# Optimization experiments

Hardware: AMD Instinct MI355X
Metric: run time of the kernel (lower is better)

The kernel has to match this reference:

```python
import jax, jax.numpy as jnp
import numpy as np

SC = 11  # window stride / block size; unfold kernel = 3*SC = 33, padding = SC


def _unfold3(x, sc):
    """Equivalent of nn.Unfold(kernel=3*sc, stride=sc, padding=sc) on [b,c,H,W]
    where H, W are multiples of sc. Returns [b, c, 9*sc*sc, n_windows].
    Patch ordering within K differs from torch by a fixed permutation, which is
    immaterial: all contractions over K (mask, softmax, value aggregation) are
    permutation-invariant as long as the same unfold is used everywhere."""
    b, c, H, W = x.shape
    h_sc, w_sc = H // sc, W // sc
    xp = jnp.pad(x, ((0, 0), (0, 0), (sc, sc), (sc, sc)))
    blk = xp.reshape(b, c, h_sc + 2, sc, w_sc + 2, sc)
    # 3x3 neighborhood of sc-blocks around each window
    pat = jnp.stack([blk[:, :, di:di + h_sc, :, dj:dj + w_sc, :]
                     for di in range(3) for dj in range(3)], axis=2)
    # [b,c,9,h_sc,r,w_sc,s] -> [b,c,9,r,s,h_sc,w_sc] -> [b,c,9*sc*sc,n]
    pat = pat.transpose(0, 1, 2, 4, 6, 3, 5)
    return pat.reshape(b, c, 9 * sc * sc, h_sc * w_sc)


def _block_q(x, sc):
    """view(b,c,h_sc,sc,w_sc,sc).permute(0,1,2,4,3,5) -> [b,c,n,sc*sc]"""
    b, c, H, W = x.shape
    h_sc, w_sc = H // sc, W // sc
    y = x.reshape(b, c, h_sc, sc, w_sc, sc).transpose(0, 1, 2, 4, 3, 5)
    return y.reshape(b, c, h_sc * w_sc, sc * sc)


def setup_inputs() -> dict:
    key = jax.random.key(0)
    k1, k2, k3, k4, k5, k6 = jax.random.split(key, 6)
    b, c, h, w = 2, 64, 256, 256
    s = 1.0 / np.sqrt(c)
    return {
        "x_key": jax.random.normal(k1, (b, c, h, w), jnp.float32),
        "x_ref": jax.random.normal(k2, (b, c, h, w), jnp.float32),
        "Wq": jax.random.normal(k3, (c, c), jnp.float32) * s,
        "Wk": jax.random.normal(k4, (c, c), jnp.float32) * s,
        "Wv": jax.random.normal(k5, (c, c), jnp.float32) * s,
        "gamma": jax.random.normal(k6, (1,), jnp.float32) * 0.1,
    }


def reference(x_key, x_ref, Wq, Wk, Wv, gamma):
    sc = SC
    b, c, h_in, w_in = x_key.shape
    x_pad = sc - w_in % sc
    y_pad = sc - h_in % sc
    pad = ((0, 0), (0, 0), (0, y_pad), (0, x_pad))
    fk = jnp.pad(x_key, pad)
    fr = jnp.pad(x_ref, pad)
    b, c, h, w = fk.shape
    h_sc, w_sc = h // sc, w // sc

    # validity mask -> additive attention bias (out-of-image keys penalized)
    fm = jnp.pad(jnp.ones((1, 1, h_in, w_in), fk.dtype), pad)
    fm_k = _unfold3(fm, sc)          # [1,1,K,n]
    fm_q = _block_q(fm, sc)          # [1,1,n,s]
    am = (jnp.einsum('bckn,bcns->bkns', fm_k, fm_q) - 1.0) * 99.0  # [1,K,n,s]

    scale = c ** (-0.5)
    q = jnp.einsum('oi,bihw->bohw', Wq, fk)
    k = jnp.einsum('oi,bihw->bohw', Wk, fr)
    v = jnp.einsum('oi,bihw->bohw', Wv, fr)

    k_u = _unfold3(k, sc) * scale    # [b,c,K,n]
    q_b = _block_q(q, sc)            # [b,c,n,s]
    attn = jnp.einsum('bckn,bcns->bkns', k_u, q_b) + am  # [b,K,n,s]
    attn = jax.nn.softmax(attn, axis=1)

    v_u = _unfold3(v, sc)            # [b,c,K,n]
    r = jnp.einsum('bkns,bckn->bcns', attn, v_u)  # [b,c,n,s]
    r = r.reshape(b, c, h_sc, w_sc, sc, sc).transpose(0, 1, 2, 4, 3, 5)
    r = r.reshape(b, c, h, w)[:, :, :h_in, :w_in]
    return x_ref + r * gamma[0]
```

## Files before the change

kernel.cpp:

```cpp
#include <hip/hip_runtime.h>


typedef unsigned short ushort_t;
typedef unsigned int   uint32;
typedef unsigned long long uint64;
typedef __attribute__((ext_vector_type(8))) short short8;
typedef __attribute__((ext_vector_type(4))) float f32x4;

#define MFMA16(a,b,c) __builtin_amdgcn_mfma_f32_16x16x32_bf16(a,b,c,0,0,0)

#if __has_builtin(__builtin_amdgcn_exp2f)
#define EXP2(x) __builtin_amdgcn_exp2f(x)
#else
#define EXP2(x) exp2f(x)
#endif
#if __has_builtin(__builtin_amdgcn_rcpf)
#define RCP(x) __builtin_amdgcn_rcpf(x)
#else
#define RCP(x) (1.0f/(x))
#endif

#define QPKT_OFF   0u
#define KPKT_OFF   18874368u
#define VPKT_OFF   37748736u

__device__ __forceinline__ ushort_t f2bf(float f){
  union { __bf16 h; ushort_t u; } c;
  c.h = (__bf16)f;
  return c.u;
}

__device__ __forceinline__ uint32 pkbf(float a, float b){
  union { __bf16 h[2]; uint32 u; } c;
  c.h[0] = (__bf16)a;
  c.h[1] = (__bf16)b;
  return c.u;
}

__device__ __forceinline__ void storeK8(ushort_t* __restrict__ base, int nt, int t,
                                        int l15, int h, f32x4 a){
  uint32 lo = pkbf(a[0], a[1]);
  uint32 hi = pkbf(a[2], a[3]);
  int lanep = l15 + 16*((2*t + (h>>1)) & 3);
  size_t off = (size_t)((nt*2 + (t>>1))*64 + lanep)*16 + 8*(h&1);
  *(uint2*)((char*)base + off) = make_uint2(lo, hi);
}

__device__ __forceinline__ short8 ldWfrag(const float* __restrict__ W, int t, int ks,
                                          int l15, int h, float scale){
  const float* p = W + (16*t + l15)*64 + 32*ks + 8*h;
  float4 a = *(const float4*)p;
  float4 b = *(const float4*)(p + 4);
  union { uint4 u; short8 s; } x;
  x.u.x = pkbf(a.x*scale, a.y*scale);
  x.u.y = pkbf(a.z*scale, a.w*scale);
  x.u.z = pkbf(b.x*scale, b.y*scale);
  x.u.w = pkbf(b.z*scale, b.w*scale);
  return x.s;
}

__global__ __launch_bounds__(256) void proj_kernel(
    const float* __restrict__ xk, const float* __restrict__ xr,
    const float* __restrict__ Wq, const float* __restrict__ Wk, const float* __restrict__ Wv,
    ushort_t* __restrict__ qpkt, ushort_t* __restrict__ kpkt, ushort_t* __restrict__ vpkt)
{
  __shared__ __align__(16) float sX[64*192];
  const int tid = threadIdx.x;
  const int lane = tid & 63, wv = tid >> 6;
  const int l15 = lane & 15, h = lane >> 4;
  const int bid = blockIdx.x;
  const bool isQ = bid >= 1152;
  const int id = isQ ? bid - 1152 : bid;
  const int b = id / 576, rem = id % 576, ty = rem / 24, tx = rem % 24;
  const float* xs = (isQ ? xk : xr) + (size_t)b*64*65536;
  const int oy = ty*11, ox = tx*11;
  const int ox3 = ox & 3, xa = ox - ox3;

  #pragma unroll
  for (int i = tid; i < 1024; i += 256) sX[(i>>4)*192 + 176 + (i&15)] = 0.f;

  {
    const int ch = tid >> 2, seg = tid & 3;
    const float* rowp = xs + (size_t)ch*65536 + (size_t)oy*256 + (xa + 4*seg);
    float* sdst = sX + ch*192 + 4*seg;
    if (ty < 23 && tx < 23){
      #pragma unroll
      for (int y = 0; y < 11; ++y)
        *(float4*)(sdst + y*16) = *(const float4*)(rowp + y*256);
    } else {
      const int xg = xa + 4*seg;
      #pragma unroll
      for (int y = 0; y < 11; ++y){
        const bool rk = (oy + y) < 256;
        float4 v;
        v.x = (rk && xg+0 < 256) ? rowp[y*256+0] : 0.f;
        v.y = (rk && xg+1 < 256) ? rowp[y*256+1] : 0.f;
        v.z = (rk && xg+2 < 256) ? rowp[y*256+2] : 0.f;
        v.w = (rk && xg+3 < 256) ? rowp[y*256+3] : 0.f;
        *(float4*)(sdst + y*16) = v;
      }
    }
  }
  __syncthreads();

  const f32x4 zero = {0.f, 0.f, 0.f, 0.f};
  #define XFL(nt, ks, dst) { \
    const int px_ = 16*(nt) + l15; \
    const int y_ = (px_*745) >> 13; \
    const float* pp_ = sX + (32*(ks) + 8*h)*192 + y_*16 + (px_ - y_*11) + ox3; \
    union { uint4 u; short8 s; } r_; \
    r_.u.x = pkbf(pp_[0],    pp_[192]); \
    r_.u.y = pkbf(pp_[384],  pp_[576]); \
    r_.u.z = pkbf(pp_[768],  pp_[960]); \
    r_.u.w = pkbf(pp_[1152], pp_[1344]); \
    dst = r_.s; }

  if (!isQ){
    short8 wkf[4][2], wvf[4][2];
    #pragma unroll
    for (int t = 0; t < 4; ++t){
      wkf[t][0] = ldWfrag(Wk, t, 0, l15, h, 1.f);  wkf[t][1] = ldWfrag(Wk, t, 1, l15, h, 1.f);
      wvf[t][0] = ldWfrag(Wv, t, 0, l15, h, 1.f);  wvf[t][1] = ldWfrag(Wv, t, 1, l15, h, 1.f);
    }
    ushort_t* kb = kpkt + (size_t)id*8192;
    ushort_t* vb = vpkt + (size_t)id*8192;
    const int nt0 = 2*wv, nt1 = 2*wv + 1;
    short8 xf0[2], xf1[2];
    XFL(nt0, 0, xf0[0]); XFL(nt0, 1, xf0[1]);
    XFL(nt1, 0, xf1[0]); XFL(nt1, 1, xf1[1]);
    #pragma unroll
    for (int t = 0; t < 4; ++t){
      f32x4 ak0 = MFMA16(wkf[t][0], xf0[0], zero); ak0 = MFMA16(wkf[t][1], xf0[1], ak0);
      f32x4 ak1 = MFMA16(wkf[t][0], xf1[0], zero); ak1 = MFMA16(wkf[t][1], xf1[1], ak1);
      f32x4 av0 = MFMA16(xf0[0], wvf[t][0], zero); av0 = MFMA16(xf0[1], wvf[t][1], av0);
      f32x4 av1 = MFMA16(xf1[0], wvf[t][0], zero); av1 = MFMA16(xf1[1], wvf[t][1], av1);
      storeK8(kb, nt0, t, l15, h, ak0);
      storeK8(kb, nt1, t, l15, h, ak1);
      uint4 pv;
      pv.x = pkbf(av0[0], av0[1]); pv.y = pkbf(av0[2], av0[3]);
      pv.z = pkbf(av1[0], av1[1]); pv.w = pkbf(av1[2], av1[3]);
      *(uint4*)((char*)vb + (size_t)((wv*4 + t)*64 + lane)*16) = pv;
    }
  } else {
    const float C1 = 0.18033688011112042f;
    short8 wqf[4][2];
    #pragma unroll
    for (int t = 0; t < 4; ++t){
      wqf[t][0] = ldWfrag(Wq, t, 0, l15, h, C1);  wqf[t][1] = ldWfrag(Wq, t, 1, l15, h, C1);
    }
    ushort_t* qb = qpkt + (size_t)id*8192;
    #pragma unroll
    for (int nn = 0; nn < 2; ++nn){
      const int nt = 2*wv + nn;
      short8 xf[2];
      XFL(nt, 0, xf[0]); XFL(nt, 1, xf[1]);
      #pragma unroll
      for (int t = 0; t < 4; ++t){
        f32x4 aq = MFMA16(wqf[t][0], xf[0], zero); aq = MFMA16(wqf[t][1], xf[1], aq);
        storeK8(qb, nt, t, l15, h, aq);
      }
    }
  }
  #undef XFL
}

__global__ __launch_bounds__(256) void attn_kernel(
    ushort_t* qpkt,
    const ushort_t* __restrict__ kpkt, const ushort_t* __restrict__ vpkt,
    const float* __restrict__ gamma)
{
  __shared__ __align__(16) char smem[49152];
  const int tid = threadIdx.x;
  const int lane = tid & 63, wave = tid >> 6;
  const int qh = wave & 1, kh = wave >> 1;
  const int win = (blockIdx.x & 7)*144 + (blockIdx.x >> 3);
  const int b = win / 576, wid = win % 576, wy = wid / 24, wx = wid % 24;
  const int l15 = lane & 15, h = lane >> 4;

  short8 qf[4][2];
  {
    const ushort_t* qblk = qpkt + (size_t)win*8192;
    #pragma unroll
    for (int mt = 0; mt < 4; ++mt){
      qf[mt][0] = *(const short8*)(qblk + (size_t)(((4*qh+mt)*2 + 0)*64 + lane)*8);
      qf[mt][1] = *(const short8*)(qblk + (size_t)(((4*qh+mt)*2 + 1)*64 + lane)*8);
    }
  }

  uint64 cks = 0; int nv = 0;
  #pragma unroll
  for (int ck = 0; ck < 9; ++ck){
    const int ty = wy - 1 + ck/3, tx = wx - 1 + ck%3;
    if ((unsigned)ty < 24u && (unsigned)tx < 24u){
      cks |= ((uint64)ck) << (4*nv); ++nv;
    }
  }
  const int nu = 2*nv;

  const f32x4 zz = {0.f,0.f,0.f,0.f};
  f32x4 o[4][4], lsumC[4];
  #pragma unroll
  for (int mt = 0; mt < 4; ++mt){
    lsumC[mt] = zz;
    #pragma unroll
    for (int u = 0; u < 4; ++u) o[mt][u] = zz;
  }
  f32x4 init_i;
  #pragma unroll
  for (int r = 0; r < 4; ++r) init_i[r] = (4*h + r >= 9) ? -1.0e4f : 0.f;
  short8 ones;
  #pragma unroll
  for (int j = 0; j < 8; ++j) ones[j] = (short)0x3F80;

  const ushort_t* gsrc = (wave < 2) ? kpkt : vpkt;
  const int ldsoff = (wave >> 1)*8192 + (wave & 1)*4096;

  #define STAGE(u, bo) { \
    const int t_ = (u) >> 1, hf_ = (u) & 1; \
    const int ck_ = (int)((cks >> (4*t_)) & 15); \
    const int cy_ = (ck_*11) >> 5; \
    const int ty_ = wy - 1 + cy_, tx_ = wx - 1 + (ck_ - 3*cy_); \
    const char* g_ = (const char*)(gsrc + (size_t)(b*576 + ty_*24 + tx_)*8192) \
                     + hf_*8192 + (wave & 1)*4096 + lane*16; \
    char* l_ = smem + (bo)*16384 + ldsoff + lane*16; \
    _Pragma("unroll") \
    for (int i_ = 0; i_ < 4; ++i_) \
      __builtin_amdgcn_global_load_lds( \
        (const __attribute__((address_space(1))) uint32*)(g_ + i_*1024), \
        (__attribute__((address_space(3))) uint32*)(l_ + i_*1024), 16, 0, 0); \
  }

  STAGE(0, 0);
  STAGE(1, 1);
  STAGE(2, 2);

  int bu = 0;
  #pragma unroll 1
  for (int u = 0; u < nu; ++u){
    const int remst = nu - 1 - u;
    if (remst >= 2)      { __asm__ volatile("s_waitcnt vmcnt(8)" ::: "memory"); }
    else if (remst == 1) { __asm__ volatile("s_waitcnt vmcnt(4)" ::: "memory"); }
    else                 { __asm__ volatile("s_waitcnt vmcnt(0)" ::: "memory"); }
    __builtin_amdgcn_s_barrier();
    __asm__ volatile("" ::: "memory");

    const int t = u >> 1, hf = u & 1;
    const int ckv = (int)((cks >> (4*t)) & 15);
    const int cyv = (ckv*11) >> 5;
    const int tyv = wy - 1 + cyv, txv = wx - 1 + (ckv - 3*cyv);
    const bool ey = (tyv == 23), ex = (txv == 23);
    const int ntp = 2*hf + kh;

    f32x4 b0, b1;
    if (ey | ex){
      #pragma unroll
      for (int kt = 0; kt < 2; ++kt){
        f32x4 bb;
        #pragma unroll
        for (int r = 0; r < 4; ++r){
          const int kl = 32*ntp + 16*kt + 4*h + r;
          const int ky = (kl*745) >> 13, kx = kl - ky*11;
          bool ok = (kl < 121) && (!ey || ky < 3) && (!ex || kx < 3);
          bb[r] = ok ? 0.f : -1.0e4f;
        }
        if (kt) b1 = bb; else b0 = bb;
      }
    } else {
      b0 = zz;
      b1 = (hf & kh) ? init_i : zz;
    }

    const char* lk = smem + bu*16384 + kh*4096;
    const char* lv = smem + bu*16384 + 8192 + kh*4096;
    short8 kf00 = *(const short8*)(lk + (0*64 + lane)*16);
    short8 kf01 = *(const short8*)(lk + (1*64 + lane)*16);
    short8 kf10 = *(const short8*)(lk + (2*64 + lane)*16);
    short8 kf11 = *(const short8*)(lk + (3*64 + lane)*16);
    short8 vf0  = *(const short8*)(lv + (0*64 + lane)*16);
    short8 vf1  = *(const short8*)(lv + (1*64 + lane)*16);
    short8 vf2  = *(const short8*)(lv + (2*64 + lane)*16);
    short8 vf3  = *(const short8*)(lv + (3*64 + lane)*16);

    __builtin_amdgcn_s_setprio(1);
    #pragma unroll
    for (int mt = 0; mt < 4; ++mt){
      f32x4 s0 = MFMA16(kf00, qf[mt][0], b0); s0 = MFMA16(kf01, qf[mt][1], s0);
      f32x4 s1 = MFMA16(kf10, qf[mt][0], b1); s1 = MFMA16(kf11, qf[mt][1], s1);
      float p[8];
      #pragma unroll
      for (int r = 0; r < 4; ++r){
        p[r]   = EXP2(s0[r]);
        p[4+r] = EXP2(s1[r]);
      }
      union { uint4 uu; short8 s; } af;
      af.uu.x = pkbf(p[0], p[1]); af.uu.y = pkbf(p[2], p[3]);
      af.uu.z = pkbf(p[4], p[5]); af.uu.w = pkbf(p[6], p[7]);
      o[mt][0] = MFMA16(af.s, vf0, o[mt][0]);
      o[mt][1] = MFMA16(af.s, vf1, o[mt][1]);
      o[mt][2] = MFMA16(af.s, vf2, o[mt][2]);
      o[mt][3] = MFMA16(af.s, vf3, o[mt][3]);
      lsumC[mt] = MFMA16(af.s, ones, lsumC[mt]);
    }
    __builtin_amdgcn_s_setprio(0);

    __asm__ volatile("" ::: "memory");
    __builtin_amdgcn_s_barrier();
    if (u + 3 < nu) STAGE(u + 3, bu);
    bu = (bu == 2) ? 0 : bu + 1;
  }
  #undef STAGE

  __syncthreads();
  {
    float* base = (float*)(smem + qh*12288);
    if (kh){
      #pragma unroll
      for (int mt = 0; mt < 4; ++mt){
        *(f32x4*)(base + (mt*2+0)*256 + lane*4) = o[mt][0];
        *(f32x4*)(base + (mt*2+1)*256 + lane*4) = o[mt][1];
        *(f32x4*)(base + (8+mt)*256 + lane*4)   = lsumC[mt];
      }
    }
  }
  __syncthreads();
  if (!kh){
    float* base = (float*)(smem + qh*12288);
    #pragma unroll
    for (int mt = 0; mt < 4; ++mt){
      o[mt][0] += *(const f32x4*)(base + (mt*2+0)*256 + lane*4);
      o[mt][1] += *(const f32x4*)(base + (mt*2+1)*256 + lane*4);
      lsumC[mt] += *(const f32x4*)(base + (8+mt)*256 + lane*4);
    }
  }
  __syncthreads();
  {
    float* base2 = (float*)(smem + qh*8192);
    if (kh){
      #pragma unroll
      for (int mt = 0; mt < 4; ++mt){
        *(f32x4*)(base2 + (mt*2+0)*256 + lane*4) = o[mt][2];
        *(f32x4*)(base2 + (mt*2+1)*256 + lane*4) = o[mt][3];
      }
    }
  }
  __syncthreads();
  if (!kh){
    float* base2 = (float*)(smem + qh*8192);
    #pragma unroll
    for (int mt = 0; mt < 4; ++mt){
      o[mt][2] += *(const f32x4*)(base2 + (mt*2+0)*256 + lane*4);
      o[mt][3] += *(const f32x4*)(base2 + (mt*2+1)*256 + lane*4);
    }
    const float gm = gamma[0];
    ushort_t* rb = qpkt + (size_t)win*8192 + (size_t)qh*4096;
    #pragma unroll
    for (int mt = 0; mt < 4; ++mt){
      #pragma unroll
      for (int r = 0; r < 4; ++r){
        const float wg = gm * RCP(lsumC[mt][r]);
        const int qs = 16*mt + 4*h + r;
        #pragma unroll
        for (int u = 0; u < 4; ++u)
          rb[(size_t)qs*64 + 16*u + l15] = f2bf(wg * o[mt][u][r]);
      }
    }
  }
}

__global__ __launch_bounds__(256) void ep_kernel(
    const float* __restrict__ xref, const ushort_t* __restrict__ rbuf,
    float* __restrict__ out)
{
  __shared__ float tile[64][65];
  const int tid = threadIdx.x;
  const int bidx = blockIdx.x;
  const int xc = bidx & 3, y = (bidx >> 2) & 255, b = bidx >> 10;
  const int wy = (y*745) >> 13, qy = y - wy*11;
  {
    const int ch = tid & 63, xs4 = tid >> 6;
    #pragma unroll
    for (int xi = 0; xi < 16; ++xi){
      const int xl = xi*4 + xs4;
      const int x = xc*64 + xl;
      const int wx = (x*745) >> 13, qx = x - wx*11;
      const size_t ridx = (size_t)(b*576 + wy*24 + wx)*8192 + (size_t)(qy*11 + qx)*64 + ch;
      tile[xl][ch] = __uint_as_float(((uint32)rbuf[ridx]) << 16);
    }
  }
  __syncthreads();
  {
    const int xl = tid & 63, cg = tid >> 6;
    const size_t base = (size_t)b*4194304 + (size_t)y*256 + xc*64 + xl;
    #pragma unroll
    for (int ci = 0; ci < 16; ++ci){
      const int c2 = ci*4 + cg;
      const size_t idx = base + (size_t)c2*65536;
      out[idx] = xref[idx] + tile[xl][c2];
    }
  }
}

extern "C" void kernel_launch(void* const* d_in, const int* in_sizes, int n_in,
                              void* d_out, int out_size, void* d_ws, size_t ws_size,
                              hipStream_t stream)
{
  const float* xk = (const float*)d_in[0];
  const float* xr = (const float*)d_in[1];
  const float* Wq = (const float*)d_in[2];
  const float* Wk = (const float*)d_in[3];
  const float* Wv = (const float*)d_in[4];
  const float* gm = (const float*)d_in[5];
  float* out = (float*)d_out;
  char* ws = (char*)d_ws;
  ushort_t* qp = (ushort_t*)(ws + QPKT_OFF);
  ushort_t* kp = (ushort_t*)(ws + KPKT_OFF);
  ushort_t* vp = (ushort_t*)(ws + VPKT_OFF);
  (void)in_sizes; (void)n_in; (void)out_size; (void)ws_size;

  proj_kernel<<<2304, 256, 0, stream>>>(xk, xr, Wq, Wk, Wv, qp, kp, vp);
  attn_kernel<<<1152, 256, 0, stream>>>(qp, kp, vp, gm);
  ep_kernel<<<2048, 256, 0, stream>>>(xr, qp, out);
}
```

Before: 236.2 us.

## Load K/V fragments directly into registers with triple-buffered register pipeline

Replaces the LDS-staged global_load_lds triple buffer, with its barriers and vmcnt waits, with per-wave direct global loads of K and V fragments into three rotating register sets. Each wave now loads only the fragments it consumes, so the per-iteration workgroup barriers go away and shared memory shrinks to the epilogue's needs. The trade-offs are higher VGPR pressure from 24 extra short8 registers, which may lower occupancy, and reliance on the compiler to place waits for the in-flight loads. Both q-half waves now fetch the same K/V tiles separately, which increases global/L2 traffic.

```diff
diff --git a/kernel.cpp b/kernel.cpp
--- a/kernel.cpp
+++ b/kernel.cpp
@@ -169,7 +169,7 @@
     const ushort_t* __restrict__ kpkt, const ushort_t* __restrict__ vpkt,
     const float* __restrict__ gamma)
 {
-  __shared__ __align__(16) char smem[49152];
+  __shared__ __align__(16) char smem[24576];
   const int tid = threadIdx.x;
   const int lane = tid & 63, wave = tid >> 6;
   const int qh = wave & 1, kh = wave >> 1;
@@ -212,103 +212,89 @@
   #pragma unroll
   for (int j = 0; j < 8; ++j) ones[j] = (short)0x3F80;
 
-  const ushort_t* gsrc = (wave < 2) ? kpkt : vpkt;
-  const int ldsoff = (wave >> 1)*8192 + (wave & 1)*4096;
-
-  #define STAGE(u, bo) { \
-    const int t_ = (u) >> 1, hf_ = (u) & 1; \
+  const int lane16 = lane*16;
+
+  #define ISSUE(KD, VD, u_) { \
+    const int t_ = (u_) >> 1, hf_ = (u_) & 1; \
     const int ck_ = (int)((cks >> (4*t_)) & 15); \
     const int cy_ = (ck_*11) >> 5; \
-    const int ty_ = wy - 1 + cy_, tx_ = wx - 1 + (ck_ - 3*cy_); \
-    const char* g_ = (const char*)(gsrc + (size_t)(b*576 + ty_*24 + tx_)*8192) \
-                     + hf_*8192 + (wave & 1)*4096 + lane*16; \
-    char* l_ = smem + (bo)*16384 + ldsoff + lane*16; \
+    const size_t tb_ = ((size_t)(b*576 + (wy-1+cy_)*24 + (wx-1+(ck_-3*cy_))) << 14) \
+                       + ((size_t)hf_ << 13) + ((size_t)kh << 12) + (size_t)lane16; \
+    const char* kg_ = (const char*)kpkt + tb_; \
+    const char* vg_ = (const char*)vpkt + tb_; \
     _Pragma("unroll") \
-    for (int i_ = 0; i_ < 4; ++i_) \
-      __builtin_amdgcn_global_load_lds( \
-        (const __attribute__((address_space(1))) uint32*)(g_ + i_*1024), \
-        (__attribute__((address_space(3))) uint32*)(l_ + i_*1024), 16, 0, 0); \
-  }
-
-  STAGE(0, 0);
-  STAGE(1, 1);
-  STAGE(2, 2);
-
-  int bu = 0;
-  #pragma unroll 1
-  for (int u = 0; u < nu; ++u){
-    const int remst = nu - 1 - u;
-    if (remst >= 2)      { __asm__ volatile("s_waitcnt vmcnt(8)" ::: "memory"); }
-    else if (remst == 1) { __asm__ volatile("s_waitcnt vmcnt(4)" ::: "memory"); }
-    else                 { __asm__ volatile("s_waitcnt vmcnt(0)" ::: "memory"); }
-    __builtin_amdgcn_s_barrier();
-    __asm__ volatile("" ::: "memory");
-
-    const int t = u >> 1, hf = u & 1;
-    const int ckv = (int)((cks >> (4*t)) & 15);
-    const int cyv = (ckv*11) >> 5;
-    const int tyv = wy - 1 + cyv, txv = wx - 1 + (ckv - 3*cyv);
-    const bool ey = (tyv == 23), ex = (txv == 23);
-    const int ntp = 2*hf + kh;
-
-    f32x4 b0, b1;
-    if (ey | ex){
-      #pragma unroll
-      for (int kt = 0; kt < 2; ++kt){
-        f32x4 bb;
-        #pragma unroll
-        for (int r = 0; r < 4; ++r){
-          const int kl = 32*ntp + 16*kt + 4*h + r;
-          const int ky = (kl*745) >> 13, kx = kl - ky*11;
-          bool ok = (kl < 121) && (!ey || ky < 3) && (!ex || kx < 3);
-          bb[r] = ok ? 0.f : -1.0e4f;
-        }
-        if (kt) b1 = bb; else b0 = bb;
-      }
-    } else {
-      b0 = zz;
-      b1 = (hf & kh) ? init_i : zz;
-    }
-
-    const char* lk = smem + bu*16384 + kh*4096;
-    const char* lv = smem + bu*16384 + 8192 + kh*4096;
-    short8 kf00 = *(const short8*)(lk + (0*64 + lane)*16);
-    short8 kf01 = *(const short8*)(lk + (1*64 + lane)*16);
-    short8 kf10 = *(const short8*)(lk + (2*64 + lane)*16);
-    short8 kf11 = *(const short8*)(lk + (3*64 + lane)*16);
-    short8 vf0  = *(const short8*)(lv + (0*64 + lane)*16);
-    short8 vf1  = *(const short8*)(lv + (1*64 + lane)*16);
-    short8 vf2  = *(const short8*)(lv + (2*64 + lane)*16);
-    short8 vf3  = *(const short8*)(lv + (3*64 + lane)*16);
-
-    __builtin_amdgcn_s_setprio(1);
-    #pragma unroll
-    for (int mt = 0; mt < 4; ++mt){
-      f32x4 s0 = MFMA16(kf00, qf[mt][0], b0); s0 = MFMA16(kf01, qf[mt][1], s0);
-      f32x4 s1 = MFMA16(kf10, qf[mt][0], b1); s1 = MFMA16(kf11, qf[mt][1], s1);
-      float p[8];
-      #pragma unroll
-      for (int r = 0; r < 4; ++r){
-        p[r]   = EXP2(s0[r]);
-        p[4+r] = EXP2(s1[r]);
-      }
-      union { uint4 uu; short8 s; } af;
-      af.uu.x = pkbf(p[0], p[1]); af.uu.y = pkbf(p[2], p[3]);
-      af.uu.z = pkbf(p[4], p[5]); af.uu.w = pkbf(p[6], p[7]);
-      o[mt][0] = MFMA16(af.s, vf0, o[mt][0]);
-      o[mt][1] = MFMA16(af.s, vf1, o[mt][1]);
-      o[mt][2] = MFMA16(af.s, vf2, o[mt][2]);
-      o[mt][3] = MFMA16(af.s, vf3, o[mt][3]);
-      lsumC[mt] = MFMA16(af.s, ones, lsumC[mt]);
-    }
-    __builtin_amdgcn_s_setprio(0);
-
-    __asm__ volatile("" ::: "memory");
-    __builtin_amdgcn_s_barrier();
-    if (u + 3 < nu) STAGE(u + 3, bu);
-    bu = (bu == 2) ? 0 : bu + 1;
-  }
-  #undef STAGE
+    for (int r_ = 0; r_ < 4; ++r_){ \
+      KD[r_] = *(const short8*)(kg_ + r_*1024); \
+      VD[r_] = *(const short8*)(vg_ + r_*1024); \
+    } }
+
+  #define COMPUTE(KC, VC, u_) { \
+    const int t_ = (u_) >> 1, hf_ = (u_) & 1; \
+    const int ckv = (int)((cks >> (4*t_)) & 15); \
+    const int cyv = (ckv*11) >> 5; \
+    const int tyv = wy - 1 + cyv, txv = wx - 1 + (ckv - 3*cyv); \
+    const bool ey = (tyv == 23), ex = (txv == 23); \
+    const int ntp = 2*hf_ + kh; \
+    f32x4 b0, b1; \
+    if (ey | ex){ \
+      _Pragma("unroll") \
+      for (int kt = 0; kt < 2; ++kt){ \
+        f32x4 bb; \
+        _Pragma("unroll") \
+        for (int r = 0; r < 4; ++r){ \
+          const int kl = 32*ntp + 16*kt + 4*h + r; \
+          const int ky = (kl*745) >> 13, kx = kl - ky*11; \
+          bool ok = (kl < 121) && (!ey || ky < 3) && (!ex || kx < 3); \
+          bb[r] = ok ? 0.f : -1.0e4f; \
+        } \
+        if (kt) b1 = bb; else b0 = bb; \
+      } \
+    } else { \
+      b0 = zz; \
+      b1 = (hf_ & kh) ? init_i : zz;    \
+    } \
+    __builtin_amdgcn_s_setprio(1); \
+    _Pragma("unroll") \
+    for (int mt = 0; mt < 4; ++mt){ \
+      f32x4 s0 = MFMA16(KC[0], qf[mt][0], b0); s0 = MFMA16(KC[1], qf[mt][1], s0); \
+      f32x4 s1 = MFMA16(KC[2], qf[mt][0], b1); s1 = MFMA16(KC[3], qf[mt][1], s1); \
+      float p[8]; \
+      _Pragma("unroll") \
+      for (int r = 0; r < 4; ++r){ \
+        p[r]   = EXP2(s0[r]); \
+        p[4+r] = EXP2(s1[r]); \
+      } \
+      union { uint4 uu; short8 s; } af; \
+      af.uu.x = pkbf(p[0], p[1]); af.uu.y = pkbf(p[2], p[3]); \
+      af.uu.z = pkbf(p[4], p[5]); af.uu.w = pkbf(p[6], p[7]); \
+      o[mt][0] = MFMA16(af.s, VC[0], o[mt][0]); \
+      o[mt][1] = MFMA16(af.s, VC[1], o[mt][1]); \
+      o[mt][2] = MFMA16(af.s, VC[2], o[mt][2]); \
+      o[mt][3] = MFMA16(af.s, VC[3], o[mt][3]); \
+      lsumC[mt] = MFMA16(af.s, ones, lsumC[mt]); \
+    } \
+    __builtin_amdgcn_s_setprio(0); }
+
+  short8 kA[4], vA[4], kB[4], vB[4], kC[4], vC[4];
+
+  ISSUE(kA, vA, 0);
+  ISSUE(kB, vB, 1);
+  ISSUE(kC, vC, 2);
+
+  {
+    int u = 0;
+    #pragma unroll 1
+    while (true){
+      COMPUTE(kA, vA, u); if (u + 3 < nu) ISSUE(kA, vA, u + 3);
+      if (++u >= nu) break;
+      COMPUTE(kB, vB, u); if (u + 3 < nu) ISSUE(kB, vB, u + 3);
+      if (++u >= nu) break;
+      COMPUTE(kC, vC, u); if (u + 3 < nu) ISSUE(kC, vC, u + 3);
+      if (++u >= nu) break;
+    }
+  }
+  #undef ISSUE
+  #undef COMPUTE
 
   __syncthreads();
   {
```

Result: slower. 251.6 us (+6.5%).
